# Kernel optimization log

Hardware: AMD Instinct MI355X
Metric: run time of the kernel (lower is better)

Reference implementation:

```python
import jax, jax.numpy as jnp
import numpy as np

B, P, ENC, DEC, ATT, EMB, V, MAXLEN = 64, 196, 2048, 1024, 1024, 1024, 10000, 20


def setup_inputs() -> dict:
    key = jax.random.key(0)
    ks = jax.random.split(key, 20)
    s = 0.02
    inp = {
        'encoder_out': jax.random.normal(ks[0], (B, 14, 14, ENC), jnp.float32),
        'encoded_captions': jax.random.randint(ks[1], (B, MAXLEN), 0, V),
        'caption_lengths': jax.random.randint(ks[2], (B, 1), 2, MAXLEN + 1).at[0, 0].set(MAXLEN),
        # embedding
        'emb_table': jax.random.uniform(ks[3], (V, EMB), jnp.float32, -0.1, 0.1),
        # attention MLP (weight_norm Linear == plain Linear math)
        'We': jax.random.normal(ks[4], (ATT, ENC)) * s,
        'be': jnp.zeros((ATT,), jnp.float32),
        'Wd': jax.random.normal(ks[5], (ATT, DEC)) * s,
        'bd': jnp.zeros((ATT,), jnp.float32),
        'Wf': jax.random.normal(ks[6], (1, ATT)) * s,
        'bf': jnp.zeros((1,), jnp.float32),
        # top_down_attention LSTMCell: input = EMB+ENC+DEC
        'W_ih1': jax.random.normal(ks[7], (4 * DEC, EMB + ENC + DEC)) * s,
        'W_hh1': jax.random.normal(ks[8], (4 * DEC, DEC)) * s,
        'b_ih1': jnp.zeros((4 * DEC,), jnp.float32),
        'b_hh1': jnp.zeros((4 * DEC,), jnp.float32),
        # language_model LSTMCell: input = ENC+DEC
        'W_ih2': jax.random.normal(ks[9], (4 * DEC, ENC + DEC)) * s,
        'W_hh2': jax.random.normal(ks[10], (4 * DEC, DEC)) * s,
        'b_ih2': jnp.zeros((4 * DEC,), jnp.float32),
        'b_hh2': jnp.zeros((4 * DEC,), jnp.float32),
        # output heads
        'Wfc1': jax.random.normal(ks[11], (V, DEC)) * s,
        'bfc1': jnp.zeros((V,), jnp.float32),
        'Wfc': jax.random.uniform(ks[12], (V, DEC), jnp.float32, -0.1, 0.1),
        'bfc': jnp.zeros((V,), jnp.float32),
    }
    return inp


def _lstm_cell(x, h, c, Wih, Whh, bih, bhh):
    g = x @ Wih.T + bih + h @ Whh.T + bhh
    i, f, gg, o = jnp.split(g, 4, axis=-1)  # torch gate order: i, f, g, o
    c2 = jax.nn.sigmoid(f) * c + jax.nn.sigmoid(i) * jnp.tanh(gg)
    h2 = jax.nn.sigmoid(o) * jnp.tanh(c2)
    return h2, c2


def _decode(encoder_out, encoded_captions, caption_lengths, emb_table,
            We, be, Wd, bd, Wf, bf,
            W_ih1, W_hh1, b_ih1, b_hh1, W_ih2, W_hh2, b_ih2, b_hh2,
            Wfc1, bfc1, Wfc, bfc):
    b = encoder_out.shape[0]
    enc = encoder_out.reshape(b, -1, encoder_out.shape[-1])  # (B,P,ENC)
    enc_mean = enc.mean(axis=1)
    cl = caption_lengths.squeeze(1)
    sort_ind = jnp.argsort(-cl)
    cl = cl[sort_ind]
    enc = enc[sort_ind]
    enc_mean = enc_mean[sort_ind]
    caps = encoded_captions[sort_ind]
    dec_len = cl - 1  # (B,)
    embeds = emb_table[caps]  # (B,T,EMB)
    Tdec = caps.shape[1] - 1
    # precompute encoder attention projection (loop-invariant, same math)
    att1 = jnp.einsum('bpe,ae->bpa', enc, We) + be  # (B,P,ATT)

    def step(carry, t):
        h1, c1, h2, c2 = carry
        active = (t < dec_len)[:, None]  # (B,1)
        x1 = jnp.concatenate([h2, enc_mean, embeds[:, t, :]], axis=1)
        h1n, c1n = _lstm_cell(x1, h1, c1, W_ih1, W_hh1, b_ih1, b_hh1)
        h1n = jnp.where(active, h1n, h1)
        c1n = jnp.where(active, c1n, c1)
        # Bahdanau attention
        att2 = h1n @ Wd.T + bd  # (B,ATT)
        e = jnp.einsum('bpa,a->bp', jax.nn.relu(att1 + att2[:, None, :]), Wf[0]) + bf[0]
        alpha = jax.nn.softmax(e, axis=1)
        awe = jnp.einsum('bpe,bp->be', enc, alpha)
        preds1 = h1n @ Wfc1.T + bfc1  # dropout is identity at eval
        x2 = jnp.concatenate([awe, h1n], axis=1)
        h2n, c2n = _lstm_cell(x2, h2, c2, W_ih2, W_hh2, b_ih2, b_hh2)
        h2n = jnp.where(active, h2n, h2)
        c2n = jnp.where(active, c2n, c2)
        preds = h2n @ Wfc.T + bfc
        preds = jnp.where(active, preds, 0.0)
        preds1 = jnp.where(active, preds1, 0.0)
        return (h1n, c1n, h2n, c2n), (preds, preds1)

    z = jnp.zeros((b, DEC), jnp.float32)
    (_, _, _, _), (pr, pr1) = jax.lax.scan(step, (z, z, z, z), jnp.arange(Tdec))
    predictions = jnp.transpose(pr, (1, 0, 2))  # (B,Tdec,V)
    predictions1 = jnp.transpose(pr1, (1, 0, 2))
    return predictions, predictions1, caps, dec_len, sort_ind


def reference(encoder_out, encoded_captions, caption_lengths, emb_table,
              We, be, Wd, bd, Wf, bf,
              W_ih1, W_hh1, b_ih1, b_hh1, W_ih2, W_hh2, b_ih2, b_hh2,
              Wfc1, bfc1, Wfc, bfc):
    return _decode(encoder_out, encoded_captions, caption_lengths, emb_table,
                   We, be, Wd, bd, Wf, bf,
                   W_ih1, W_hh1, b_ih1, b_hh1, W_ih2, W_hh2, b_ih2, b_hh2,
                   Wfc1, bfc1, Wfc, bfc)
```

## Files before the change

### kernel.cpp

```cpp
#include <hip/hip_runtime.h>
#include <cmath>

#define B_ 64
#define P_ 196
#define ENC_ 2048
#define DEC_ 1024
#define V_ 10000
#define MAXLEN_ 20
#define TDEC_ 19

typedef __attribute__((ext_vector_type(8))) short bf16x8;
typedef __attribute__((ext_vector_type(4))) float f32x4;


__device__ __align__(16) short g_encb[(size_t)12544 * 2048];
__device__ __align__(16) short g_encbt[(size_t)12544 * 2048];
__device__ __align__(16) short g_att1[(size_t)12544 * 1024];
__device__ __align__(16) short g_Wp1t[(size_t)4096 * 2048];
__device__ __align__(16) short g_Wemt[(size_t)4096 * 2048];
__device__ __align__(16) short g_Wembt[(size_t)4096 * 1024];
__device__ __align__(16) short g_Wc2t[(size_t)4096 * 4096];
__device__ __align__(16) short g_Webt[(size_t)1024 * 2048];
__device__ __align__(16) short g_Wdt[(size_t)1024 * 1024];
__device__ __align__(16) short g_Wfc1t[(size_t)10000 * 1024];
__device__ __align__(16) short g_Wfct[(size_t)10000 * 1024];
__device__ __align__(16) short g_xs1[(size_t)20 * 64 * 2048];
__device__ __align__(16) short g_xemb[(size_t)19 * 64 * 1024];
__device__ __align__(16) short g_xc2[(size_t)20 * 64 * 4096];
__device__ __align__(16) short g_em[64 * 2048];
__device__ __align__(16) float g_preemb[(size_t)19 * 64 * 4096];
__device__ __align__(16) float g_preem[64 * 4096];
__device__ __align__(16) float g_part[(size_t)8 * 64 * 4096];
__device__ __align__(16) float g_att2p[(size_t)4 * 64 * 1024];
__device__ __align__(16) float g_e[64 * P_];
__device__ __align__(16) float g_c1[64 * 1024];
__device__ __align__(16) float g_c2[64 * 1024];
__device__ int g_ibuf[64 + 64 + 64 * MAXLEN_];

__device__ __forceinline__ short f2b(float f) {
  unsigned u = __float_as_uint(f);
  u += 0x7FFFu + ((u >> 16) & 1u);
  return (short)(u >> 16);
}
__device__ __forceinline__ float b2f(short s) {
  return __uint_as_float(((unsigned)(unsigned short)s) << 16);
}

__global__ void k_sort(const int* __restrict__ cl_in, const int* __restrict__ caps_in,
                       int* __restrict__ sind, int* __restrict__ declen, int* __restrict__ caps_s,
                       float* __restrict__ out_caps, float* __restrict__ out_declen,
                       float* __restrict__ out_sind) {
  int i = threadIdx.x;
  __shared__ int cl[B_];
  cl[i] = cl_in[i];
  __syncthreads();
  int my = cl[i], pos = 0;
  for (int j = 0; j < B_; ++j) {
    int cj = cl[j];
    if (cj > my || (cj == my && j < i)) pos++;
  }
  sind[pos] = i;
  __syncthreads();
  int sb = sind[i];
  int dl = cl[sb] - 1;
  declen[i] = dl;
  out_declen[i] = (float)dl;
  out_sind[i] = (float)sb;
  for (int t = 0; t < MAXLEN_; ++t) {
    int v = caps_in[sb * MAXLEN_ + t];
    caps_s[i * MAXLEN_ + t] = v;
    out_caps[i * MAXLEN_ + t] = (float)v;
  }
}

__global__ __launch_bounds__(256) void k_encprep(const float* __restrict__ enc,
                                                 const int* __restrict__ sind,
                                                 short* __restrict__ encb,
                                                 short* __restrict__ encbt) {
  int mg = blockIdx.x;
  int b = mg / P_, p = mg - b * P_;
  int tid = threadIdx.x;
  const float* src = enc + ((size_t)sind[b] * P_ + p) * ENC_ + tid * 8;
  float4 a = *(const float4*)src;
  float4 c = *(const float4*)(src + 4);
  bf16x8 v;
  v[0] = f2b(a.x); v[1] = f2b(a.y); v[2] = f2b(a.z); v[3] = f2b(a.w);
  v[4] = f2b(c.x); v[5] = f2b(c.y); v[6] = f2b(c.z); v[7] = f2b(c.w);
  *(bf16x8*)(encb + (size_t)mg * ENC_ + tid * 8) = v;
  size_t off = (((size_t)(mg >> 4) * 64 + (tid >> 2)) << 9) +
               (((mg & 15) | ((tid & 3) << 4)) << 3);
  *(bf16x8*)(encbt + off) = v;
}

__global__ __launch_bounds__(256) void k_encmeanb(const short* __restrict__ encb,
                                                  short* __restrict__ em) {
  int b = blockIdx.x;
  int col0 = threadIdx.x * 8;
  const short* src = encb + (size_t)b * P_ * ENC_ + col0;
  float acc[8] = {};
  for (int p = 0; p < P_; ++p) {
    bf16x8 v = *(const bf16x8*)(src + (size_t)p * ENC_);
#pragma unroll
    for (int j = 0; j < 8; ++j) acc[j] += b2f(v[j]);
  }
#pragma unroll
  for (int j = 0; j < 8; ++j) em[b * 2048 + col0 + j] = f2b(acc[j] * (1.0f / 196.0f));
}

__global__ __launch_bounds__(256) void k_prefill(const float* __restrict__ emb,
                                                 const int* __restrict__ caps_s,
                                                 short* __restrict__ xemb) {
  int t = blockIdx.x, b = blockIdx.y, tid = threadIdx.x;
  short* xr = xemb + ((size_t)t * 64 + b) * 1024;
  int cap = caps_s[b * MAXLEN_ + t];
  int j = tid * 4;
  float4 v = *(const float4*)(emb + (size_t)cap * 1024 + j);
  short4 o;
  o.x = f2b(v.x); o.y = f2b(v.y); o.z = f2b(v.z); o.w = f2b(v.w);
  *(short4*)(xr + j) = o;
}

__global__ void k_f2bts(const float* __restrict__ src, int Kstride, int c0, int ncols,
                        short* __restrict__ dst, int Ktot, int koff) {
  int idx = blockIdx.x * 256 + threadIdx.x;
  int kc = ncols >> 3;
  int r = idx / kc, k8 = (idx - r * kc) << 3;
  const float* s = src + (size_t)r * Kstride + c0 + k8;
  float4 a = *(const float4*)s;
  float4 c = *(const float4*)(s + 4);
  bf16x8 v;
  v[0] = f2b(a.x); v[1] = f2b(a.y); v[2] = f2b(a.z); v[3] = f2b(a.w);
  v[4] = f2b(c.x); v[5] = f2b(c.y); v[6] = f2b(c.z); v[7] = f2b(c.w);
  int kg = koff + k8;
  size_t off = (((size_t)(r >> 4) * (Ktot >> 5) + (kg >> 5)) << 9) +
               (((r & 15) | (((kg >> 3) & 3) << 4)) << 3);
  *(bf16x8*)(dst + off) = v;
}

__global__ __launch_bounds__(1024) void k_att1_t(const short* __restrict__ At,
                                                 const short* __restrict__ Wt,
                                                 const float* __restrict__ be,
                                                 short* __restrict__ Cb) {
  int wave = threadIdx.x >> 6, lane = threadIdx.x & 63;
  int mt0 = blockIdx.x * 8 + (wave >> 3) * 4;
  int nt0 = blockIdx.y * 32 + (wave & 7) * 4;
  f32x4 acc[4][4] = {};
  const short* Ab = At + ((size_t)mt0 * 64 << 9) + lane * 8;
  const short* Wb = Wt + ((size_t)nt0 * 64 << 9) + lane * 8;
  for (int kt = 0; kt < 64; ++kt) {
    bf16x8 a[4], b[4];
#pragma unroll
    for (int i = 0; i < 4; ++i) a[i] = *(const bf16x8*)(Ab + (((size_t)i * 64 + kt) << 9));
#pragma unroll
    for (int j = 0; j < 4; ++j) b[j] = *(const bf16x8*)(Wb + (((size_t)j * 64 + kt) << 9));
#pragma unroll
    for (int i = 0; i < 4; ++i)
#pragma unroll
      for (int j = 0; j < 4; ++j)
        acc[i][j] = __builtin_amdgcn_mfma_f32_16x16x32_bf16(a[i], b[j], acc[i][j], 0, 0, 0);
  }
  int rr = (lane >> 4) * 4, cc = lane & 15;
  int m0 = mt0 * 16, n0 = nt0 * 16;
#pragma unroll
  for (int i = 0; i < 4; ++i)
#pragma unroll
    for (int j = 0; j < 4; ++j) {
      int n = n0 + j * 16 + cc;
      float bn = be[n];
#pragma unroll
      for (int r = 0; r < 4; ++r) {
        int m = m0 + i * 16 + rr + r;
        Cb[(size_t)m * 1024 + n] = f2b(acc[i][j][r] + bn);
      }
    }
}

__global__ __launch_bounds__(256) void k_skinny_t(const short* __restrict__ A, int lda,
                                                  const short* __restrict__ Wt, int ldw,
                                                  int N, int kchunk, float* __restrict__ part) {
  int wave = threadIdx.x >> 6, lane = threadIdx.x & 63;
  int n0 = blockIdx.x * 128 + wave * 32;
  int kb = blockIdx.y * kchunk;
  int lr = lane & 15, lk = (lane >> 4) * 8;
  int ntk = ldw >> 5;
  int nt0 = n0 >> 4;
  f32x4 acc[4][2] = {};
  const short* Ab = A + (size_t)lr * lda + kb + lk;
  const short* Wb0 = Wt + (((size_t)nt0 * ntk + (kb >> 5)) << 9) + lane * 8;
  const short* Wb1 = Wt + (((size_t)(nt0 + 1) * ntk + (kb >> 5)) << 9) + lane * 8;
  int nkt = kchunk >> 5;
  for (int kt = 0; kt < nkt; ++kt) {
    bf16x8 a[4], b0, b1;
#pragma unroll
    for (int i = 0; i < 4; ++i) a[i] = *(const bf16x8*)(Ab + (size_t)i * 16 * lda + kt * 32);
    b0 = *(const bf16x8*)(Wb0 + ((size_t)kt << 9));
    b1 = *(const bf16x8*)(Wb1 + ((size_t)kt << 9));
#pragma unroll
    for (int i = 0; i < 4; ++i) {
      acc[i][0] = __builtin_amdgcn_mfma_f32_16x16x32_bf16(a[i], b0, acc[i][0], 0, 0, 0);
      acc[i][1] = __builtin_amdgcn_mfma_f32_16x16x32_bf16(a[i], b1, acc[i][1], 0, 0, 0);
    }
  }
  float* po = part + (size_t)blockIdx.y * 64 * N;
  int rr = (lane >> 4) * 4, cc = lane & 15;
#pragma unroll
  for (int i = 0; i < 4; ++i)
#pragma unroll
    for (int j = 0; j < 2; ++j) {
      int n = n0 + j * 16 + cc;
#pragma unroll
      for (int r = 0; r < 4; ++r) {
        int m = i * 16 + rr + r;
        po[(size_t)m * N + n] = acc[i][j][r];
      }
    }
}

__global__ void k_sumn(const float* __restrict__ part, int nsplit, float* __restrict__ dst) {
  int idx = blockIdx.x * 256 + threadIdx.x;
  float s = 0.0f;
  for (int q = 0; q < nsplit; ++q) s += part[(size_t)q * 64 * 4096 + idx];
  dst[idx] = s;
}

__global__ __launch_bounds__(256) void k_mid_emb4(const short* __restrict__ xemb,
                                                  const short* __restrict__ Wt,
                                                  float* __restrict__ preemb) {
  int t = blockIdx.x;
  const short* A = xemb + (size_t)t * 64 * 1024;
  int wave = threadIdx.x >> 6, lane = threadIdx.x & 63;
  int nt0 = blockIdx.y * 16 + wave * 4;
  int lr = lane & 15, lk = (lane >> 4) * 8;
  f32x4 acc[4][4] = {};
  const short* Ab = A + (size_t)lr * 1024 + lk;
  const short* Wb[4];
#pragma unroll
  for (int j = 0; j < 4; ++j) Wb[j] = Wt + ((size_t)(nt0 + j) * 32 << 9) + lane * 8;
  for (int kt = 0; kt < 32; ++kt) {
    bf16x8 a[4], b[4];
#pragma unroll
    for (int j = 0; j < 4; ++j) b[j] = *(const bf16x8*)(Wb[j] + ((size_t)kt << 9));
#pragma unroll
    for (int i = 0; i < 4; ++i) a[i] = *(const bf16x8*)(Ab + (size_t)i * 16 * 1024 + kt * 32);
#pragma unroll
    for (int i = 0; i < 4; ++i)
#pragma unroll
      for (int j = 0; j < 4; ++j)
        acc[i][j] = __builtin_amdgcn_mfma_f32_16x16x32_bf16(a[i], b[j], acc[i][j], 0, 0, 0);
  }
  float* po = preemb + (size_t)t * 64 * 4096;
  int rr = (lane >> 4) * 4, cc = lane & 15;
#pragma unroll
  for (int i = 0; i < 4; ++i)
#pragma unroll
    for (int j = 0; j < 4; ++j) {
      int n = (nt0 + j) * 16 + cc;
#pragma unroll
      for (int r = 0; r < 4; ++r) {
        int m = i * 16 + rr + r;
        po[(size_t)m * 4096 + n] = acc[i][j][r];
      }
    }
}

__global__ void k_gates(const float* __restrict__ part, int nsplit,
                        const float* __restrict__ pre, const float* __restrict__ pre2,
                        const float* __restrict__ bih, const float* __restrict__ bhh,
                        float* __restrict__ c,
                        const short* __restrict__ hold, int ldo,
                        short* __restrict__ dst1, int ld1,
                        short* __restrict__ dst2, int ld2,
                        const int* __restrict__ declen, int t) {
  int idx = blockIdx.x * 256 + threadIdx.x;
  int b = idx >> 10, j = idx & 1023;
  const float* pb = part + (size_t)b * 4096;
  float gi = bih[j] + bhh[j];
  float gf = bih[1024 + j] + bhh[1024 + j];
  float gg = bih[2048 + j] + bhh[2048 + j];
  float go = bih[3072 + j] + bhh[3072 + j];
  if (pre) {
    const float* pp = pre + (size_t)b * 4096;
    gi += pp[j]; gf += pp[j + 1024]; gg += pp[j + 2048]; go += pp[j + 3072];
  }
  if (pre2) {
    const float* pp = pre2 + (size_t)b * 4096;
    gi += pp[j]; gf += pp[j + 1024]; gg += pp[j + 2048]; go += pp[j + 3072];
  }
  for (int s = 0; s < nsplit; ++s) {
    const float* p = pb + (size_t)s * 64 * 4096;
    gi += p[j]; gf += p[j + 1024]; gg += p[j + 2048]; go += p[j + 3072];
  }
  float si = 1.0f / (1.0f + expf(-gi));
  float sf = 1.0f / (1.0f + expf(-gf));
  float so = 1.0f / (1.0f + expf(-go));
  float cn = sf * c[idx] + si * tanhf(gg);
  float hn = so * tanhf(cn);
  short hb;
  if (t < declen[b]) {
    c[idx] = cn;
    hb = f2b(hn);
  } else {
    hb = hold[b * ldo + j];
  }
  dst1[b * ld1 + j] = hb;
  dst2[b * ld2 + j] = hb;
}

__global__ __launch_bounds__(256) void k_e(const short* __restrict__ att1,
                                           const float* __restrict__ att2p,
                                           const float* __restrict__ bd,
                                           const float* __restrict__ Wf,
                                           const float* __restrict__ bf,
                                           float* __restrict__ e) {
  __shared__ float a2[1024];
  int b = blockIdx.x / 49, pq = blockIdx.x % 49;
  for (int i = threadIdx.x; i < 1024; i += 256) {
    float s = bd[i];
#pragma unroll
    for (int q = 0; q < 4; ++q) s += att2p[q * 65536 + b * 1024 + i];
    a2[i] = s;
  }
  __syncthreads();
  int wave = threadIdx.x >> 6, lane = threadIdx.x & 63;
  int p = pq * 4 + wave;
  const short* a1 = att1 + ((size_t)(b * P_ + p)) * 1024;
  float s = 0.0f;
#pragma unroll
  for (int h = 0; h < 2; ++h) {
    int k0 = lane * 8 + h * 512;
    bf16x8 v = *(const bf16x8*)(a1 + k0);
#pragma unroll
    for (int j = 0; j < 8; ++j) s += Wf[k0 + j] * fmaxf(b2f(v[j]) + a2[k0 + j], 0.0f);
  }
#pragma unroll
  for (int off = 32; off; off >>= 1) s += __shfl_down(s, off);
  if (lane == 0) e[b * P_ + p] = s + bf[0];
}

__global__ __launch_bounds__(256) void k_sawe(const float* __restrict__ e,
                                              const short* __restrict__ encb,
                                              short* __restrict__ xc2t) {
  int b = blockIdx.x, ch = blockIdx.y;
  __shared__ float al[P_];
  __shared__ float red[8][256];
  int tid = threadIdx.x;
  if (tid < 64) {
    float vals[4];
    float mx = -1e30f;
#pragma unroll
    for (int q = 0; q < 4; ++q) {
      int p = tid + q * 64;
      vals[q] = (p < P_) ? e[b * P_ + p] : -1e30f;
      mx = fmaxf(mx, vals[q]);
    }
#pragma unroll
    for (int off = 32; off; off >>= 1) mx = fmaxf(mx, __shfl_xor(mx, off));
    float sum = 0.0f;
#pragma unroll
    for (int q = 0; q < 4; ++q) {
      int p = tid + q * 64;
      vals[q] = (p < P_) ? expf(vals[q] - mx) : 0.0f;
      sum += vals[q];
    }
#pragma unroll
    for (int off = 32; off; off >>= 1) sum += __shfl_xor(sum, off);
    float inv = 1.0f / sum;
#pragma unroll
    for (int q = 0; q < 4; ++q) {
      int p = tid + q * 64;
      if (p < P_) al[p] = vals[q] * inv;
    }
  }
  __syncthreads();
  int pg = tid >> 5, cg = tid & 31;
  int col = ch * 256 + cg * 8;
  const short* src = encb + (size_t)b * P_ * ENC_ + col;
  float acc[8] = {};
  for (int p = pg; p < P_; p += 8) {
    bf16x8 v = *(const bf16x8*)(src + (size_t)p * ENC_);
    float ap = al[p];
#pragma unroll
    for (int j = 0; j < 8; ++j) acc[j] += ap * b2f(v[j]);
  }
#pragma unroll
  for (int j = 0; j < 8; ++j) red[pg][cg * 8 + j] = acc[j];
  __syncthreads();
  float s = 0.0f;
#pragma unroll
  for (int g = 0; g < 8; ++g) s += red[g][tid];
  xc2t[b * 4096 + ch * 256 + tid] = f2b(s);
}

__global__ __launch_bounds__(256) void k_head4(const short* __restrict__ Aall,
                                               const short* __restrict__ Wt,
                                               const float* __restrict__ bias,
                                               float* __restrict__ outp,
                                               const int* __restrict__ declen) {
  int t = blockIdx.x;
  const short* A = Aall + (size_t)t * (64 * 4096);
  int wave = threadIdx.x >> 6, lane = threadIdx.x & 63;
  int nt0 = blockIdx.y * 16 + wave * 4;
  int lr = lane & 15, lk = (lane >> 4) * 8;
  f32x4 acc[4][4] = {};
  const short* Ab = A + (size_t)lr * 4096 + lk;
  const short* Wb[4];
  bool ok[4];
#pragma unroll
  for (int j = 0; j < 4; ++j) {
    ok[j] = (nt0 + j) < (V_ >> 4);
    Wb[j] = Wt + ((size_t)(ok[j] ? nt0 + j : 0) * 32 << 9) + lane * 8;
  }
  for (int kt = 0; kt < 32; ++kt) {
    bf16x8 a[4], b[4];
#pragma unroll
    for (int j = 0; j < 4; ++j) b[j] = *(const bf16x8*)(Wb[j] + ((size_t)kt << 9));
#pragma unroll
    for (int i = 0; i < 4; ++i) a[i] = *(const bf16x8*)(Ab + (size_t)i * 16 * 4096 + kt * 32);
#pragma unroll
    for (int i = 0; i < 4; ++i)
#pragma unroll
      for (int j = 0; j < 4; ++j)
        acc[i][j] = __builtin_amdgcn_mfma_f32_16x16x32_bf16(a[i], b[j], acc[i][j], 0, 0, 0);
  }
  int rr = (lane >> 4) * 4, cc = lane & 15;
#pragma unroll
  for (int j = 0; j < 4; ++j) {
    if (!ok[j]) continue;
    int n = (nt0 + j) * 16 + cc;
    float bn = bias[n];
#pragma unroll
    for (int i = 0; i < 4; ++i) {
#pragma unroll
      for (int r = 0; r < 4; ++r) {
        int b = i * 16 + rr + r;
        float val = acc[i][j][r] + bn;
        outp[((size_t)b * TDEC_ + t) * V_ + n] = (t < declen[b]) ? val : 0.0f;
      }
    }
  }
}

extern "C" void kernel_launch(void* const* d_in, const int* in_sizes, int n_in,
                              void* d_out, int out_size, void* d_ws, size_t ws_size,
                              hipStream_t stream) {
  (void)in_sizes; (void)n_in; (void)d_ws; (void)ws_size; (void)out_size;
  const float* enc  = (const float*)d_in[0];
  const int*   caps = (const int*)d_in[1];
  const int*   cl   = (const int*)d_in[2];
  const float* emb  = (const float*)d_in[3];
  const float* We   = (const float*)d_in[4];
  const float* be   = (const float*)d_in[5];
  const float* Wd   = (const float*)d_in[6];
  const float* bd   = (const float*)d_in[7];
  const float* Wf   = (const float*)d_in[8];
  const float* bf   = (const float*)d_in[9];
  const float* Wih1 = (const float*)d_in[10];
  const float* Whh1 = (const float*)d_in[11];
  const float* bih1 = (const float*)d_in[12];
  const float* bhh1 = (const float*)d_in[13];
  const float* Wih2 = (const float*)d_in[14];
  const float* Whh2 = (const float*)d_in[15];
  const float* bih2 = (const float*)d_in[16];
  const float* bhh2 = (const float*)d_in[17];
  const float* Wfc1 = (const float*)d_in[18];
  const float* bfc1 = (const float*)d_in[19];
  const float* Wfc  = (const float*)d_in[20];
  const float* bfc  = (const float*)d_in[21];
  float* out = (float*)d_out;

  short *encb, *encbt, *att1, *Wp1t, *Wemt, *Wembt, *Wc2t, *Webt, *Wdt, *Wfc1t, *Wfct;
  short *xs1, *xemb, *xc2, *em;
  float *preemb, *preem, *part, *att2p, *e, *c1, *c2;
  int* ib;
  hipGetSymbolAddress((void**)&encb, HIP_SYMBOL(g_encb));
  hipGetSymbolAddress((void**)&encbt, HIP_SYMBOL(g_encbt));
  hipGetSymbolAddress((void**)&att1, HIP_SYMBOL(g_att1));
  hipGetSymbolAddress((void**)&Wp1t, HIP_SYMBOL(g_Wp1t));
  hipGetSymbolAddress((void**)&Wemt, HIP_SYMBOL(g_Wemt));
  hipGetSymbolAddress((void**)&Wembt, HIP_SYMBOL(g_Wembt));
  hipGetSymbolAddress((void**)&Wc2t, HIP_SYMBOL(g_Wc2t));
  hipGetSymbolAddress((void**)&Webt, HIP_SYMBOL(g_Webt));
  hipGetSymbolAddress((void**)&Wdt, HIP_SYMBOL(g_Wdt));
  hipGetSymbolAddress((void**)&Wfc1t, HIP_SYMBOL(g_Wfc1t));
  hipGetSymbolAddress((void**)&Wfct, HIP_SYMBOL(g_Wfct));
  hipGetSymbolAddress((void**)&xs1, HIP_SYMBOL(g_xs1));
  hipGetSymbolAddress((void**)&xemb, HIP_SYMBOL(g_xemb));
  hipGetSymbolAddress((void**)&xc2, HIP_SYMBOL(g_xc2));
  hipGetSymbolAddress((void**)&em, HIP_SYMBOL(g_em));
  hipGetSymbolAddress((void**)&preemb, HIP_SYMBOL(g_preemb));
  hipGetSymbolAddress((void**)&preem, HIP_SYMBOL(g_preem));
  hipGetSymbolAddress((void**)&part, HIP_SYMBOL(g_part));
  hipGetSymbolAddress((void**)&att2p, HIP_SYMBOL(g_att2p));
  hipGetSymbolAddress((void**)&e, HIP_SYMBOL(g_e));
  hipGetSymbolAddress((void**)&c1, HIP_SYMBOL(g_c1));
  hipGetSymbolAddress((void**)&c2, HIP_SYMBOL(g_c2));
  hipGetSymbolAddress((void**)&ib, HIP_SYMBOL(g_ibuf));
  int* sind = ib;
  int* declen = ib + 64;
  int* caps_s = ib + 128;

  float* out_preds  = out;
  float* out_preds1 = out + (size_t)B_ * TDEC_ * V_;
  float* out_caps   = out + 2ull * B_ * TDEC_ * V_;
  float* out_declen = out_caps + B_ * MAXLEN_;
  float* out_sind   = out_declen + B_;

  k_sort<<<1, 64, 0, stream>>>(cl, caps, sind, declen, caps_s, out_caps, out_declen, out_sind);
  hipMemsetAsync(c1, 0, 64 * 1024 * sizeof(float), stream);
  hipMemsetAsync(c2, 0, 64 * 1024 * sizeof(float), stream);
  hipMemsetAsync(xs1, 0, (size_t)64 * 2048 * sizeof(short), stream);
  hipMemsetAsync(xc2, 0, (size_t)64 * 4096 * sizeof(short), stream);
  k_encprep<<<12544, 256, 0, stream>>>(enc, sind, encb, encbt);
  k_encmeanb<<<64, 256, 0, stream>>>(encb, em);
  k_prefill<<<dim3(19, 64), 256, 0, stream>>>(emb, caps_s, xemb);
  k_f2bts<<<2048, 256, 0, stream>>>(Wih1, 4096, 0, 1024, Wp1t, 2048, 0);
  k_f2bts<<<2048, 256, 0, stream>>>(Whh1, 1024, 0, 1024, Wp1t, 2048, 1024);
  k_f2bts<<<4096, 256, 0, stream>>>(Wih1, 4096, 1024, 2048, Wemt, 2048, 0);
  k_f2bts<<<2048, 256, 0, stream>>>(Wih1, 4096, 3072, 1024, Wembt, 1024, 0);
  k_f2bts<<<6144, 256, 0, stream>>>(Wih2, 3072, 0, 3072, Wc2t, 4096, 0);
  k_f2bts<<<2048, 256, 0, stream>>>(Whh2, 1024, 0, 1024, Wc2t, 4096, 3072);
  k_f2bts<<<1024, 256, 0, stream>>>(We, 2048, 0, 2048, Webt, 2048, 0);
  k_f2bts<<<512, 256, 0, stream>>>(Wd, 1024, 0, 1024, Wdt, 1024, 0);
  k_f2bts<<<5000, 256, 0, stream>>>(Wfc1, 1024, 0, 1024, Wfc1t, 1024, 0);
  k_f2bts<<<5000, 256, 0, stream>>>(Wfc, 1024, 0, 1024, Wfct, 1024, 0);
  k_att1_t<<<dim3(98, 2), 1024, 0, stream>>>(encbt, Webt, be, att1);
  k_skinny_t<<<dim3(32, 4), 256, 0, stream>>>(em, 2048, Wemt, 2048, 4096, 512, part);
  k_sumn<<<1024, 256, 0, stream>>>(part, 4, preem);
  k_mid_emb4<<<dim3(19, 16), 256, 0, stream>>>(xemb, Wembt, preemb);

  for (int t = 0; t < TDEC_; ++t) {
    short* s1t = xs1 + (size_t)t * 64 * 2048;
    short* s1n = xs1 + (size_t)(t + 1) * 64 * 2048;
    short* x2t = xc2 + (size_t)t * 64 * 4096;
    short* x2n = xc2 + (size_t)(t + 1) * 64 * 4096;
    k_skinny_t<<<dim3(32, 8), 256, 0, stream>>>(s1t, 2048, Wp1t, 2048, 4096, 256, part);
    k_gates<<<256, 256, 0, stream>>>(part, 8, preemb + (size_t)t * 64 * 4096, preem,
                                     bih1, bhh1, c1, s1t + 1024, 2048,
                                     s1n + 1024, 2048, x2t + 2048, 4096, declen, t);
    k_skinny_t<<<dim3(8, 4), 256, 0, stream>>>(x2t + 2048, 4096, Wdt, 1024, 1024, 256, att2p);
    k_e<<<3136, 256, 0, stream>>>(att1, att2p, bd, Wf, bf, e);
    k_sawe<<<dim3(64, 8), 256, 0, stream>>>(e, encb, x2t);
    k_skinny_t<<<dim3(32, 8), 256, 0, stream>>>(x2t, 4096, Wc2t, 4096, 4096, 512, part);
    k_gates<<<256, 256, 0, stream>>>(part, 8, nullptr, nullptr, bih2, bhh2, c2, s1t, 2048,
                                     s1n, 2048, x2n + 3072, 4096, declen, t);
  }
  k_head4<<<dim3(19, 40), 256, 0, stream>>>(xc2 + 2048, Wfc1t, bfc1, out_preds1, declen);
  k_head4<<<dim3(19, 40), 256, 0, stream>>>(xc2 + 64 * 4096 + 3072, Wfct, bfc, out_preds, declen);
}
```

Before: 1.865 ms.

## Raise grid parallelism across split-K GEMMs, attention sum, and att1 tiles

Doubles the split-K factor of the recurrent skinny GEMMs (to 16 and 8 partitions) and the column split of the attention-weighted sum kernel, so the per-timestep kernels launch more blocks on the many-CU GPU. Adds a separate reduction kernel for the att2 partials so the energy kernel no longer re-sums partials in each of its 3136 blocks. The att1 GEMM moves to 256-thread blocks with smaller tiles and more of them. The cost is more partial-sum traffic in the gate kernels, one extra launch per step, and less register reuse per att1 wave.

```diff
diff --git a/kernel.cpp b/kernel.cpp
--- a/kernel.cpp
+++ b/kernel.cpp
@@ -30,8 +30,9 @@
 __device__ __align__(16) short g_em[64 * 2048];
 __device__ __align__(16) float g_preemb[(size_t)19 * 64 * 4096];
 __device__ __align__(16) float g_preem[64 * 4096];
-__device__ __align__(16) float g_part[(size_t)8 * 64 * 4096];
-__device__ __align__(16) float g_att2p[(size_t)4 * 64 * 1024];
+__device__ __align__(16) float g_part[(size_t)16 * 64 * 4096];
+__device__ __align__(16) float g_att2p[(size_t)8 * 64 * 1024];
+__device__ __align__(16) float g_att2s[64 * 1024];
 __device__ __align__(16) float g_e[64 * P_];
 __device__ __align__(16) float g_c1[64 * 1024];
 __device__ __align__(16) float g_c2[64 * 1024];
@@ -137,35 +138,35 @@
   *(bf16x8*)(dst + off) = v;
 }
 
-__global__ __launch_bounds__(1024) void k_att1_t(const short* __restrict__ At,
-                                                 const short* __restrict__ Wt,
-                                                 const float* __restrict__ be,
-                                                 short* __restrict__ Cb) {
+__global__ __launch_bounds__(256) void k_att1_t(const short* __restrict__ At,
+                                                const short* __restrict__ Wt,
+                                                const float* __restrict__ be,
+                                                short* __restrict__ Cb) {
   int wave = threadIdx.x >> 6, lane = threadIdx.x & 63;
-  int mt0 = blockIdx.x * 8 + (wave >> 3) * 4;
-  int nt0 = blockIdx.y * 32 + (wave & 7) * 4;
-  f32x4 acc[4][4] = {};
+  int mt0 = blockIdx.x * 2;
+  int nt0 = blockIdx.y * 16 + wave * 4;
+  f32x4 acc[2][4] = {};
   const short* Ab = At + ((size_t)mt0 * 64 << 9) + lane * 8;
   const short* Wb = Wt + ((size_t)nt0 * 64 << 9) + lane * 8;
   for (int kt = 0; kt < 64; ++kt) {
-    bf16x8 a[4], b[4];
-#pragma unroll
-    for (int i = 0; i < 4; ++i) a[i] = *(const bf16x8*)(Ab + (((size_t)i * 64 + kt) << 9));
+    bf16x8 a[2], b[4];
+#pragma unroll
+    for (int i = 0; i < 2; ++i) a[i] = *(const bf16x8*)(Ab + (((size_t)i * 64 + kt) << 9));
 #pragma unroll
     for (int j = 0; j < 4; ++j) b[j] = *(const bf16x8*)(Wb + (((size_t)j * 64 + kt) << 9));
 #pragma unroll
-    for (int i = 0; i < 4; ++i)
+    for (int i = 0; i < 2; ++i)
 #pragma unroll
       for (int j = 0; j < 4; ++j)
         acc[i][j] = __builtin_amdgcn_mfma_f32_16x16x32_bf16(a[i], b[j], acc[i][j], 0, 0, 0);
   }
   int rr = (lane >> 4) * 4, cc = lane & 15;
-  int m0 = mt0 * 16, n0 = nt0 * 16;
-#pragma unroll
-  for (int i = 0; i < 4; ++i)
+  int m0 = mt0 * 16;
+#pragma unroll
+  for (int i = 0; i < 2; ++i)
 #pragma unroll
     for (int j = 0; j < 4; ++j) {
-      int n = n0 + j * 16 + cc;
+      int n = (nt0 + j) * 16 + cc;
       float bn = be[n];
 #pragma unroll
       for (int r = 0; r < 4; ++r) {
@@ -221,6 +222,16 @@
   float s = 0.0f;
   for (int q = 0; q < nsplit; ++q) s += part[(size_t)q * 64 * 4096 + idx];
   dst[idx] = s;
+}
+
+__global__ void k_suma(const float* __restrict__ att2p, const float* __restrict__ bd,
+                       float* __restrict__ att2s) {
+  int idx = blockIdx.x * 256 + threadIdx.x;
+  int j = idx & 1023;
+  float s = bd[j];
+#pragma unroll
+  for (int q = 0; q < 8; ++q) s += att2p[(size_t)q * 65536 + idx];
+  att2s[idx] = s;
 }
 
 __global__ __launch_bounds__(256) void k_mid_emb4(const short* __restrict__ xemb,
@@ -307,19 +318,13 @@
 }
 
 __global__ __launch_bounds__(256) void k_e(const short* __restrict__ att1,
-                                           const float* __restrict__ att2p,
-                                           const float* __restrict__ bd,
+                                           const float* __restrict__ att2s,
                                            const float* __restrict__ Wf,
                                            const float* __restrict__ bf,
                                            float* __restrict__ e) {
   __shared__ float a2[1024];
   int b = blockIdx.x / 49, pq = blockIdx.x % 49;
-  for (int i = threadIdx.x; i < 1024; i += 256) {
-    float s = bd[i];
-#pragma unroll
-    for (int q = 0; q < 4; ++q) s += att2p[q * 65536 + b * 1024 + i];
-    a2[i] = s;
-  }
+  for (int i = threadIdx.x; i < 1024; i += 256) a2[i] = att2s[b * 1024 + i];
   __syncthreads();
   int wave = threadIdx.x >> 6, lane = threadIdx.x & 63;
   int p = pq * 4 + wave;
@@ -342,7 +347,7 @@
                                               short* __restrict__ xc2t) {
   int b = blockIdx.x, ch = blockIdx.y;
   __shared__ float al[P_];
-  __shared__ float red[8][256];
+  __shared__ float red[16][128];
   int tid = threadIdx.x;
   if (tid < 64) {
     float vals[4];
@@ -372,11 +377,11 @@
     }
   }
   __syncthreads();
-  int pg = tid >> 5, cg = tid & 31;
-  int col = ch * 256 + cg * 8;
+  int pg = tid >> 4, cg = tid & 15;
+  int col = ch * 128 + cg * 8;
   const short* src = encb + (size_t)b * P_ * ENC_ + col;
   float acc[8] = {};
-  for (int p = pg; p < P_; p += 8) {
+  for (int p = pg; p < P_; p += 16) {
     bf16x8 v = *(const bf16x8*)(src + (size_t)p * ENC_);
     float ap = al[p];
 #pragma unroll
@@ -385,10 +390,12 @@
 #pragma unroll
   for (int j = 0; j < 8; ++j) red[pg][cg * 8 + j] = acc[j];
   __syncthreads();
-  float s = 0.0f;
-#pragma unroll
-  for (int g = 0; g < 8; ++g) s += red[g][tid];
-  xc2t[b * 4096 + ch * 256 + tid] = f2b(s);
+  if (tid < 128) {
+    float s = 0.0f;
+#pragma unroll
+    for (int g = 0; g < 16; ++g) s += red[g][tid];
+    xc2t[b * 4096 + ch * 128 + tid] = f2b(s);
+  }
 }
 
 __global__ __launch_bounds__(256) void k_head4(const short* __restrict__ Aall,
@@ -470,7 +477,7 @@
 
   short *encb, *encbt, *att1, *Wp1t, *Wemt, *Wembt, *Wc2t, *Webt, *Wdt, *Wfc1t, *Wfct;
   short *xs1, *xemb, *xc2, *em;
-  float *preemb, *preem, *part, *att2p, *e, *c1, *c2;
+  float *preemb, *preem, *part, *att2p, *att2s, *e, *c1, *c2;
   int* ib;
   hipGetSymbolAddress((void**)&encb, HIP_SYMBOL(g_encb));
   hipGetSymbolAddress((void**)&encbt, HIP_SYMBOL(g_encbt));
@@ -491,6 +498,7 @@
   hipGetSymbolAddress((void**)&preem, HIP_SYMBOL(g_preem));
   hipGetSymbolAddress((void**)&part, HIP_SYMBOL(g_part));
   hipGetSymbolAddress((void**)&att2p, HIP_SYMBOL(g_att2p));
+  hipGetSymbolAddress((void**)&att2s, HIP_SYMBOL(g_att2s));
   hipGetSymbolAddress((void**)&e, HIP_SYMBOL(g_e));
   hipGetSymbolAddress((void**)&c1, HIP_SYMBOL(g_c1));
   hipGetSymbolAddress((void**)&c2, HIP_SYMBOL(g_c2));
@@ -523,7 +531,7 @@
   k_f2bts<<<512, 256, 0, stream>>>(Wd, 1024, 0, 1024, Wdt, 1024, 0);
   k_f2bts<<<5000, 256, 0, stream>>>(Wfc1, 1024, 0, 1024, Wfc1t, 1024, 0);
   k_f2bts<<<5000, 256, 0, stream>>>(Wfc, 1024, 0, 1024, Wfct, 1024, 0);
-  k_att1_t<<<dim3(98, 2), 1024, 0, stream>>>(encbt, Webt, be, att1);
+  k_att1_t<<<dim3(392, 4), 256, 0, stream>>>(encbt, Webt, be, att1);
   k_skinny_t<<<dim3(32, 4), 256, 0, stream>>>(em, 2048, Wemt, 2048, 4096, 512, part);
   k_sumn<<<1024, 256, 0, stream>>>(part, 4, preem);
   k_mid_emb4<<<dim3(19, 16), 256, 0, stream>>>(xemb, Wembt, preemb);
@@ -533,15 +541,16 @@
     short* s1n = xs1 + (size_t)(t + 1) * 64 * 2048;
     short* x2t = xc2 + (size_t)t * 64 * 4096;
     short* x2n = xc2 + (size_t)(t + 1) * 64 * 4096;
-    k_skinny_t<<<dim3(32, 8), 256, 0, stream>>>(s1t, 2048, Wp1t, 2048, 4096, 256, part);
-    k_gates<<<256, 256, 0, stream>>>(part, 8, preemb + (size_t)t * 64 * 4096, preem,
+    k_skinny_t<<<dim3(32, 16), 256, 0, stream>>>(s1t, 2048, Wp1t, 2048, 4096, 128, part);
+    k_gates<<<256, 256, 0, stream>>>(part, 16, preemb + (size_t)t * 64 * 4096, preem,
                                      bih1, bhh1, c1, s1t + 1024, 2048,
                                      s1n + 1024, 2048, x2t + 2048, 4096, declen, t);
-    k_skinny_t<<<dim3(8, 4), 256, 0, stream>>>(x2t + 2048, 4096, Wdt, 1024, 1024, 256, att2p);
-    k_e<<<3136, 256, 0, stream>>>(att1, att2p, bd, Wf, bf, e);
-    k_sawe<<<dim3(64, 8), 256, 0, stream>>>(e, encb, x2t);
-    k_skinny_t<<<dim3(32, 8), 256, 0, stream>>>(x2t, 4096, Wc2t, 4096, 4096, 512, part);
-    k_gates<<<256, 256, 0, stream>>>(part, 8, nullptr, nullptr, bih2, bhh2, c2, s1t, 2048,
+    k_skinny_t<<<dim3(8, 8), 256, 0, stream>>>(x2t + 2048, 4096, Wdt, 1024, 1024, 128, att2p);
+    k_suma<<<256, 256, 0, stream>>>(att2p, bd, att2s);
+    k_e<<<3136, 256, 0, stream>>>(att1, att2s, Wf, bf, e);
+    k_sawe<<<dim3(64, 16), 256, 0, stream>>>(e, encb, x2t);
+    k_skinny_t<<<dim3(32, 16), 256, 0, stream>>>(x2t, 4096, Wc2t, 4096, 4096, 256, part);
+    k_gates<<<256, 256, 0, stream>>>(part, 16, nullptr, nullptr, bih2, bhh2, c2, s1t, 2048,
                                      s1n, 2048, x2n + 3072, 4096, declen, t);
   }
   k_head4<<<dim3(19, 40), 256, 0, stream>>>(xc2 + 2048, Wfc1t, bfc1, out_preds1, declen);
```

Measured after the change: 1.987 ms. +6.5%, slower.
